# Optimization experiments

Measured on AMD Instinct MI355X. Metric: run time of the kernel, lower is better.

## Reference

```python
import jax, jax.numpy as jnp
import numpy as np

B, L, E, S = 4, 1024, 256, 32  # batch, seq_len, e_dim, local window half-size
NEG = -1e30  # stands in for excluding out-of-range positions from softmax


def setup_inputs() -> dict:
    key = jax.random.key(0)
    ks = jax.random.split(key, 8)
    sc = 1.0 / np.sqrt(E)
    return {
        "q": jax.random.normal(ks[0], (B, L, E), jnp.float32),
        "Wq": jax.random.normal(ks[1], (E, E), jnp.float32) * sc,
        "bq": jax.random.normal(ks[2], (E,), jnp.float32) * sc,
        "Wk": jax.random.normal(ks[3], (E, E), jnp.float32) * sc,
        "bk": jax.random.normal(ks[4], (E,), jnp.float32) * sc,
        "Wv": jax.random.normal(ks[5], (E, E), jnp.float32) * sc,
        "bv": jax.random.normal(ks[6], (E,), jnp.float32) * sc,
        "pos_bias": jax.random.normal(ks[7], (2 * S + 1, E), jnp.float32),
    }


def reference(q, Wq, bq, Wk, bk, Wv, bv, pos_bias):
    # Linear projections (nn.Linear: x @ W.T + b)
    Q = q @ Wq.T + bq
    K = q @ Wk.T + bk
    V = q @ Wv.T + bv

    W = 2 * S + 1
    rel = jnp.arange(-S, S + 1)                      # [W] relative offsets
    idx = jnp.arange(L)[:, None] + rel[None, :]       # [L, W] absolute positions
    valid = (idx >= 0) & (idx < L)                    # in-sequence window entries
    idxc = jnp.clip(idx, 0, L - 1)
    strict = jnp.abs(rel) < S                         # |j-i| < s mask (zeroes K at edges)

    # Gather windows: [B, L, W, E]
    K_win = K[:, idxc] + pos_bias[rel + S][None, None, :, :]
    K_masked = jnp.where(strict[None, None, :, None], K_win, 0.0)
    # Out-of-range positions excluded from softmax entirely (logit -> -inf)
    logits = jnp.where(valid[None, :, :, None], Q[:, :, None, :] * K_masked, NEG)
    weights = jax.nn.softmax(logits, axis=2)          # per-channel softmax over window

    V_win = jnp.where(valid[None, :, :, None], V[:, idxc], 0.0)
    ctx = jnp.sum(weights * V_win, axis=2)            # [B, L, E]

    sig = jax.nn.sigmoid(Q)
    # sigmoid applied inside the loop and again at the end -> squared
    return sig * sig * ctx
```

## Files before the change

kernel.cpp:

```cpp
#include <hip/hip_runtime.h>
#include <hip/hip_bf16.h>

#define B_ 4
#define L_ 1024
#define E_ 256
#define S_ 32

typedef __bf16 bf16x8 __attribute__((ext_vector_type(8)));
typedef float f32x4 __attribute__((ext_vector_type(4)));

__device__ __forceinline__ __bf16 bf_from_bits(unsigned short u) {
    __bf16 b;
    __builtin_memcpy(&b, &u, 2);
    return b;
}

__device__ __forceinline__ void load8split(const float* __restrict__ p,
                                           bf16x8& h, bf16x8& l) {
    const float4 x0 = *(const float4*)p;
    const float4 x1 = *(const float4*)(p + 4);
    const float xs[8] = {x0.x, x0.y, x0.z, x0.w, x1.x, x1.y, x1.z, x1.w};
#pragma unroll
    for (int j = 0; j < 8; ++j) {
        const unsigned hb = __float_as_uint(xs[j]) & 0xFFFF0000u;
        h[j] = bf_from_bits((unsigned short)(hb >> 16));
        l[j] = (__bf16)(xs[j] - __uint_as_float(hb));
    }
}

__global__ __launch_bounds__(256, 1) void qkv_gemm2(
    const float* __restrict__ A,
    const float* __restrict__ Wq, const float* __restrict__ bq,
    const float* __restrict__ Wk, const float* __restrict__ bk,
    const float* __restrict__ Wv, const float* __restrict__ bv,
    float* __restrict__ Qo, float* __restrict__ Ko, float* __restrict__ Vo)
{
    const float* Wm;
    const float* bm;
    float* Om;
    const int z = blockIdx.z;
    if (z == 0)      { Wm = Wq; bm = bq; Om = Qo; }
    else if (z == 1) { Wm = Wk; bm = bk; Om = Ko; }
    else             { Wm = Wv; bm = bv; Om = Vo; }

    const int wave = threadIdx.x >> 6;
    const int lane = threadIdx.x & 63;
    const int rsel = lane & 15;
    const int koff = (lane >> 4) * 8;

    const int m0 = blockIdx.x * 32;
    const int nb = wave * 64;

    const float* pa0 = A + (size_t)(m0 + rsel) * 256 + koff;
    const float* pa1 = pa0 + (size_t)16 * 256;
    const float* pw0 = Wm + (size_t)(nb + 0  + rsel) * 256 + koff;
    const float* pw1 = Wm + (size_t)(nb + 16 + rsel) * 256 + koff;
    const float* pw2 = Wm + (size_t)(nb + 32 + rsel) * 256 + koff;
    const float* pw3 = Wm + (size_t)(nb + 48 + rsel) * 256 + koff;

    f32x4 acc[2][4];
#pragma unroll
    for (int mt = 0; mt < 2; ++mt)
#pragma unroll
        for (int nt = 0; nt < 4; ++nt)
            acc[mt][nt] = (f32x4){0.f, 0.f, 0.f, 0.f};

#pragma unroll
    for (int k0 = 0; k0 < 256; k0 += 32) {
        bf16x8 ah[2], al[2], bh[4], bl[4];
        load8split(pa0 + k0, ah[0], al[0]);
        load8split(pa1 + k0, ah[1], al[1]);
        load8split(pw0 + k0, bh[0], bl[0]);
        load8split(pw1 + k0, bh[1], bl[1]);
        load8split(pw2 + k0, bh[2], bl[2]);
        load8split(pw3 + k0, bh[3], bl[3]);
#pragma unroll
        for (int mt = 0; mt < 2; ++mt)
#pragma unroll
            for (int nt = 0; nt < 4; ++nt) {
                acc[mt][nt] = __builtin_amdgcn_mfma_f32_16x16x32_bf16(
                    ah[mt], bh[nt], acc[mt][nt], 0, 0, 0);
                acc[mt][nt] = __builtin_amdgcn_mfma_f32_16x16x32_bf16(
                    ah[mt], bl[nt], acc[mt][nt], 0, 0, 0);
                acc[mt][nt] = __builtin_amdgcn_mfma_f32_16x16x32_bf16(
                    al[mt], bh[nt], acc[mt][nt], 0, 0, 0);
            }
    }

#pragma unroll
    for (int mt = 0; mt < 2; ++mt) {
        const int mrow = m0 + mt * 16 + (lane >> 4) * 4;
#pragma unroll
        for (int nt = 0; nt < 4; ++nt) {
            const int n = nb + nt * 16 + rsel;
            const float bias = bm[n];
#pragma unroll
            for (int r = 0; r < 4; ++r)
                Om[(size_t)(mrow + r) * 256 + n] = acc[mt][nt][r] + bias;
        }
    }
}

#define TI2 32
#define CH2 64
#define HB2 96
#define PS2 68

__global__ __launch_bounds__(256) void aft_stage2b(
    const float* __restrict__ Q, const float* __restrict__ K,
    const float* __restrict__ V, const float* __restrict__ pb,
    float* __restrict__ out)
{
    __shared__ float Kw[HB2][PS2];
    __shared__ float Vw[HB2][PS2];
    __shared__ float Pw[2 * S_ + 1][PS2];

    const int tid = threadIdx.x;
    const int b  = blockIdx.y;
    const int i0 = blockIdx.x * TI2;
    const int c0 = blockIdx.z * CH2;

    const float* Kb = K + (size_t)b * L_ * E_;
    const float* Vb = V + (size_t)b * L_ * E_;

    for (int idx = tid; idx < HB2 * 16; idx += 256) {
        const int r  = idx >> 4;
        const int cq = (idx & 15) * 4;
        int j = i0 - S_ + r;
        j = j < 0 ? 0 : (j > L_ - 1 ? L_ - 1 : j);
        const size_t g = (size_t)j * E_ + c0 + cq;
        *(float4*)&Kw[r][cq] = *(const float4*)(Kb + g);
        *(float4*)&Vw[r][cq] = *(const float4*)(Vb + g);
    }
    for (int idx = tid; idx < (2 * S_ + 1) * 16; idx += 256) {
        const int r  = idx >> 4;
        const int cq = (idx & 15) * 4;
        *(float4*)&Pw[r][cq] = *(const float4*)(pb + (size_t)r * E_ + c0 + cq);
    }
    __syncthreads();

    const int cq = (tid & 15) * 4;
    const int is = tid >> 4;

#pragma unroll
    for (int rep = 0; rep < 2; ++rep) {
        const int rr = is + rep * 16;
        const int i  = i0 + rr;

        const float4 qv = *(const float4*)(Q + ((size_t)b * L_ + i) * E_ + c0 + cq);

        float den0 = 0.f, den1 = 0.f, den2 = 0.f, den3 = 0.f;
        float num0 = 0.f, num1 = 0.f, num2 = 0.f, num3 = 0.f;

        const int jlo = (i - S_ < 0) ? 0 : (i - S_);
        const int jhi = (i + S_ > L_ - 1) ? (L_ - 1) : (i + S_);

        for (int j = jlo; j <= jhi; ++j) {
            const int r = j - (i0 - S_);
            const int w = j - i + S_;
            const float4 vv = *(const float4*)&Vw[r][cq];

            float kx = 0.f, ky = 0.f, kz = 0.f, kw = 0.f;
            if (w != 0 && w != 2 * S_) {
                const float4 kk = *(const float4*)&Kw[r][cq];
                const float4 pp = *(const float4*)&Pw[w][cq];
                kx = kk.x + pp.x;
                ky = kk.y + pp.y;
                kz = kk.z + pp.z;
                kw = kk.w + pp.w;
            }
            const float e0 = __expf(qv.x * kx);
            const float e1 = __expf(qv.y * ky);
            const float e2 = __expf(qv.z * kz);
            const float e3 = __expf(qv.w * kw);
            den0 += e0; den1 += e1; den2 += e2; den3 += e3;
            num0 += e0 * vv.x; num1 += e1 * vv.y;
            num2 += e2 * vv.z; num3 += e3 * vv.w;
        }

        const float s0 = 1.f / (1.f + __expf(-qv.x));
        const float s1 = 1.f / (1.f + __expf(-qv.y));
        const float s2 = 1.f / (1.f + __expf(-qv.z));
        const float s3 = 1.f / (1.f + __expf(-qv.w));

        float4 o;
        o.x = s0 * s0 * num0 / den0;
        o.y = s1 * s1 * num1 / den1;
        o.z = s2 * s2 * num2 / den2;
        o.w = s3 * s3 * num3 / den3;
        *(float4*)(out + ((size_t)b * L_ + i) * E_ + c0 + cq) = o;
    }
}

#define TI 32
#define CG 64
#define RK 96
#define LDP 68

__global__ __launch_bounds__(256) void aft_fused(
    const float* __restrict__ q,
    const float* __restrict__ Wq, const float* __restrict__ bq,
    const float* __restrict__ Wk, const float* __restrict__ bk,
    const float* __restrict__ Wv, const float* __restrict__ bv,
    const float* __restrict__ pb,
    float* __restrict__ out)
{
    __shared__ float Kl[RK][LDP];
    __shared__ float Vl[RK][LDP];
    __shared__ float Ql[TI][LDP];

    const int i0 = blockIdx.x * TI;
    const int b  = blockIdx.y;
    const int c0 = blockIdx.z * CG;

    const int wave = threadIdx.x >> 6;
    const int lane = threadIdx.x & 63;
    const int rsel = lane & 15;
    const int koff = (lane >> 4) * 8;

    const float* qb = q + (size_t)b * L_ * E_;

    for (int job = wave; job < 56; job += 4) {
        int p, rt, ct;
        if (job < 24)      { p = 0; rt = job >> 2;        ct = job & 3; }
        else if (job < 48) { p = 1; rt = (job - 24) >> 2; ct = (job - 24) & 3; }
        else               { p = 2; rt = (job - 48) >> 2; ct = (job - 48) & 3; }

        int jrow = (p == 2) ? (i0 + rt * 16 + rsel)
                            : (i0 - S_ + rt * 16 + rsel);
        int jc = jrow < 0 ? 0 : (jrow > L_ - 1 ? L_ - 1 : jrow);
        const float* pa = qb + (size_t)jc * E_ + koff;

        const float* Wm = (p == 0) ? Wk : (p == 1) ? Wv : Wq;
        const float* bm = (p == 0) ? bk : (p == 1) ? bv : bq;
        const int n = c0 + ct * 16 + rsel;
        const float* pw = Wm + (size_t)n * E_ + koff;

        f32x4 acc = {0.f, 0.f, 0.f, 0.f};
#pragma unroll
        for (int k0 = 0; k0 < 256; k0 += 32) {
            bf16x8 ah, al, bh, bl;
            load8split(pa + k0, ah, al);
            load8split(pw + k0, bh, bl);
            acc = __builtin_amdgcn_mfma_f32_16x16x32_bf16(ah, bh, acc, 0, 0, 0);
            acc = __builtin_amdgcn_mfma_f32_16x16x32_bf16(ah, bl, acc, 0, 0, 0);
            acc = __builtin_amdgcn_mfma_f32_16x16x32_bf16(al, bh, acc, 0, 0, 0);
        }

        const float bias = bm[n];
        const int row0 = rt * 16 + (lane >> 4) * 4;
        const int colc = ct * 16 + rsel;
        float* dst = (p == 0) ? &Kl[0][0] : (p == 1) ? &Vl[0][0] : &Ql[0][0];
#pragma unroll
        for (int r = 0; r < 4; ++r)
            dst[(size_t)(row0 + r) * LDP + colc] = acc[r] + bias;
    }
    __syncthreads();

    const int cq  = threadIdx.x & 15;
    const int is0 = threadIdx.x >> 4;
    const int cL  = cq * 4;
    const int cG  = c0 + cL;
    const float* pbc = pb + cG;

    for (int rr = is0; rr < TI; rr += 16) {
        const int i = i0 + rr;
        const float4 qv = *(const float4*)&Ql[rr][cL];

        float den0 = 0.f, den1 = 0.f, den2 = 0.f, den3 = 0.f;
        float num0 = 0.f, num1 = 0.f, num2 = 0.f, num3 = 0.f;

        const int jlo = (i - S_ < 0) ? 0 : (i - S_);
        const int jhi = (i + S_ > L_ - 1) ? (L_ - 1) : (i + S_);

        for (int j = jlo; j <= jhi; ++j) {
            const int r = j - (i0 - S_);
            const int w = j - i + S_;
            const float4 vv = *(const float4*)&Vl[r][cL];

            float kx = 0.f, ky = 0.f, kz = 0.f, kw = 0.f;
            if (w != 0 && w != 2 * S_) {
                const float4 kk = *(const float4*)&Kl[r][cL];
                const float4 pp = *(const float4*)(pbc + (size_t)w * E_);
                kx = kk.x + pp.x;
                ky = kk.y + pp.y;
                kz = kk.z + pp.z;
                kw = kk.w + pp.w;
            }
            const float e0 = __expf(qv.x * kx);
            const float e1 = __expf(qv.y * ky);
            const float e2 = __expf(qv.z * kz);
            const float e3 = __expf(qv.w * kw);
            den0 += e0; den1 += e1; den2 += e2; den3 += e3;
            num0 += e0 * vv.x; num1 += e1 * vv.y;
            num2 += e2 * vv.z; num3 += e3 * vv.w;
        }

        const float s0 = 1.f / (1.f + __expf(-qv.x));
        const float s1 = 1.f / (1.f + __expf(-qv.y));
        const float s2 = 1.f / (1.f + __expf(-qv.z));
        const float s3 = 1.f / (1.f + __expf(-qv.w));

        float4 o;
        o.x = s0 * s0 * num0 / den0;
        o.y = s1 * s1 * num1 / den1;
        o.z = s2 * s2 * num2 / den2;
        o.w = s3 * s3 * num3 / den3;
        *(float4*)(out + ((size_t)b * L_ + i) * E_ + cG) = o;
    }
}

extern "C" void kernel_launch(void* const* d_in, const int* in_sizes, int n_in,
                              void* d_out, int out_size, void* d_ws, size_t ws_size,
                              hipStream_t stream) {
    const float* q  = (const float*)d_in[0];
    const float* Wq = (const float*)d_in[1];
    const float* bq = (const float*)d_in[2];
    const float* Wk = (const float*)d_in[3];
    const float* bk = (const float*)d_in[4];
    const float* Wv = (const float*)d_in[5];
    const float* bv = (const float*)d_in[6];
    const float* pb = (const float*)d_in[7];

    const size_t needA = (size_t)3 * 4096 * 256 * sizeof(float);

    if (ws_size >= needA) {
        float* Qf = (float*)d_ws;
        float* Kf = Qf + (size_t)4096 * 256;
        float* Vf = Kf + (size_t)4096 * 256;
        qkv_gemm2<<<dim3(128, 1, 3), 256, 0, stream>>>(q, Wq, bq, Wk, bk, Wv, bv,
                                                       Qf, Kf, Vf);
        aft_stage2b<<<dim3(L_ / TI2, B_, E_ / CH2), 256, 0, stream>>>(
            Qf, Kf, Vf, pb, (float*)d_out);
    } else {
        aft_fused<<<dim3(L_ / TI, B_, E_ / CG), 256, 0, stream>>>(
            q, Wq, bq, Wk, bk, Wv, bv, pb, (float*)d_out);
    }
}
```

Measured before the change: 124.4 us.

## Hoist strict-edge terms out of window loop and halve channel tile

The attention stage now handles the two edge window entries (w=0 and w=2S), whose masked K gives exp(0)=1, in closed form before the loop. An interior fast path then iterates only over the strict window with no per-iteration branch or bounds check, while edge rows take a masked path. The channel tile is halved so each thread handles one row, giving twice as many blocks, less LDS per block and a launch-bounds occupancy hint. The cost is reloading K/V halos across more blocks.

New measurement: 119.2 us. 1.04x faster.

```diff
diff --git a/kernel.cpp b/kernel.cpp
--- a/kernel.cpp
+++ b/kernel.cpp
@@ -101,95 +101,106 @@
     }
 }
 
-#define TI2 32
-#define CH2 64
-#define HB2 96
-#define PS2 68
-
-__global__ __launch_bounds__(256) void aft_stage2b(
+#define TI3 32
+#define CH3 32
+#define HB3 96
+#define PS3 36
+
+__global__ __launch_bounds__(256, 4) void aft_stage2c(
     const float* __restrict__ Q, const float* __restrict__ K,
     const float* __restrict__ V, const float* __restrict__ pb,
     float* __restrict__ out)
 {
-    __shared__ float Kw[HB2][PS2];
-    __shared__ float Vw[HB2][PS2];
-    __shared__ float Pw[2 * S_ + 1][PS2];
+    __shared__ float Kw[HB3][PS3];
+    __shared__ float Vw[HB3][PS3];
+    __shared__ float Pw[2 * S_ + 1][PS3];
 
     const int tid = threadIdx.x;
     const int b  = blockIdx.y;
-    const int i0 = blockIdx.x * TI2;
-    const int c0 = blockIdx.z * CH2;
+    const int i0 = blockIdx.x * TI3;
+    const int c0 = blockIdx.z * CH3;
+
+    const int cq = (tid & 7) * 4;
+    const int rr = tid >> 3;
+    const int i  = i0 + rr;
+
+    const float4 qv = *(const float4*)(Q + ((size_t)b * L_ + i) * E_ + c0 + cq);
 
     const float* Kb = K + (size_t)b * L_ * E_;
     const float* Vb = V + (size_t)b * L_ * E_;
 
-    for (int idx = tid; idx < HB2 * 16; idx += 256) {
-        const int r  = idx >> 4;
-        const int cq = (idx & 15) * 4;
+    for (int idx = tid; idx < HB3 * 8; idx += 256) {
+        const int r = idx >> 3;
+        const int c = (idx & 7) * 4;
         int j = i0 - S_ + r;
         j = j < 0 ? 0 : (j > L_ - 1 ? L_ - 1 : j);
-        const size_t g = (size_t)j * E_ + c0 + cq;
-        *(float4*)&Kw[r][cq] = *(const float4*)(Kb + g);
-        *(float4*)&Vw[r][cq] = *(const float4*)(Vb + g);
-    }
-    for (int idx = tid; idx < (2 * S_ + 1) * 16; idx += 256) {
-        const int r  = idx >> 4;
-        const int cq = (idx & 15) * 4;
-        *(float4*)&Pw[r][cq] = *(const float4*)(pb + (size_t)r * E_ + c0 + cq);
+        const size_t g = (size_t)j * E_ + c0 + c;
+        *(float4*)&Kw[r][c] = *(const float4*)(Kb + g);
+        *(float4*)&Vw[r][c] = *(const float4*)(Vb + g);
+    }
+    for (int idx = tid; idx < (2 * S_ + 1) * 8; idx += 256) {
+        const int r = idx >> 3;
+        const int c = (idx & 7) * 4;
+        *(float4*)&Pw[r][c] = *(const float4*)(pb + (size_t)r * E_ + c0 + c);
     }
     __syncthreads();
 
-    const int cq = (tid & 15) * 4;
-    const int is = tid >> 4;
-
-#pragma unroll
-    for (int rep = 0; rep < 2; ++rep) {
-        const int rr = is + rep * 16;
-        const int i  = i0 + rr;
-
-        const float4 qv = *(const float4*)(Q + ((size_t)b * L_ + i) * E_ + c0 + cq);
-
-        float den0 = 0.f, den1 = 0.f, den2 = 0.f, den3 = 0.f;
-        float num0 = 0.f, num1 = 0.f, num2 = 0.f, num3 = 0.f;
-
-        const int jlo = (i - S_ < 0) ? 0 : (i - S_);
-        const int jhi = (i + S_ > L_ - 1) ? (L_ - 1) : (i + S_);
-
-        for (int j = jlo; j <= jhi; ++j) {
-            const int r = j - (i0 - S_);
-            const int w = j - i + S_;
+    const float mA = (i >= S_) ? 1.f : 0.f;
+    const float mB = (i <= L_ - 1 - S_) ? 1.f : 0.f;
+    const float4 vA = *(const float4*)&Vw[rr][cq];
+    const float4 vB = *(const float4*)&Vw[rr + 2 * S_][cq];
+
+    float den0 = mA + mB, den1 = mA + mB, den2 = mA + mB, den3 = mA + mB;
+    float num0 = mA * vA.x + mB * vB.x;
+    float num1 = mA * vA.y + mB * vB.y;
+    float num2 = mA * vA.z + mB * vB.z;
+    float num3 = mA * vA.w + mB * vB.w;
+
+    if (i >= S_ - 1 && i <= L_ - S_) {
+#pragma unroll 7
+        for (int w = 1; w < 2 * S_; ++w) {
+            const int r = rr + w;
+            const float4 kk = *(const float4*)&Kw[r][cq];
+            const float4 pp = *(const float4*)&Pw[w][cq];
             const float4 vv = *(const float4*)&Vw[r][cq];
-
-            float kx = 0.f, ky = 0.f, kz = 0.f, kw = 0.f;
-            if (w != 0 && w != 2 * S_) {
-                const float4 kk = *(const float4*)&Kw[r][cq];
-                const float4 pp = *(const float4*)&Pw[w][cq];
-                kx = kk.x + pp.x;
-                ky = kk.y + pp.y;
-                kz = kk.z + pp.z;
-                kw = kk.w + pp.w;
-            }
-            const float e0 = __expf(qv.x * kx);
-            const float e1 = __expf(qv.y * ky);
-            const float e2 = __expf(qv.z * kz);
-            const float e3 = __expf(qv.w * kw);
+            const float e0 = __expf(qv.x * (kk.x + pp.x));
+            const float e1 = __expf(qv.y * (kk.y + pp.y));
+            const float e2 = __expf(qv.z * (kk.z + pp.z));
+            const float e3 = __expf(qv.w * (kk.w + pp.w));
             den0 += e0; den1 += e1; den2 += e2; den3 += e3;
             num0 += e0 * vv.x; num1 += e1 * vv.y;
             num2 += e2 * vv.z; num3 += e3 * vv.w;
         }
-
-        const float s0 = 1.f / (1.f + __expf(-qv.x));
-        const float s1 = 1.f / (1.f + __expf(-qv.y));
-        const float s2 = 1.f / (1.f + __expf(-qv.z));
-        const float s3 = 1.f / (1.f + __expf(-qv.w));
-
-        float4 o;
-        o.x = s0 * s0 * num0 / den0;
-        o.y = s1 * s1 * num1 / den1;
-        o.z = s2 * s2 * num2 / den2;
-        o.w = s3 * s3 * num3 / den3;
-        *(float4*)(out + ((size_t)b * L_ + i) * E_ + c0 + cq) = o;
-    }
+    } else {
+#pragma unroll 7
+        for (int w = 1; w < 2 * S_; ++w) {
+            const int r = rr + w;
+            const int j = i - S_ + w;
+            const float m = (j >= 0 && j <= L_ - 1) ? 1.f : 0.f;
+            const float4 kk = *(const float4*)&Kw[r][cq];
+            const float4 pp = *(const float4*)&Pw[w][cq];
+            const float4 vv = *(const float4*)&Vw[r][cq];
+            const float e0 = m * __expf(qv.x * (kk.x + pp.x));
+            const float e1 = m * __expf(qv.y * (kk.y + pp.y));
+            const float e2 = m * __expf(qv.z * (kk.z + pp.z));
+            const float e3 = m * __expf(qv.w * (kk.w + pp.w));
+            den0 += e0; den1 += e1; den2 += e2; den3 += e3;
+            num0 += e0 * vv.x; num1 += e1 * vv.y;
+            num2 += e2 * vv.z; num3 += e3 * vv.w;
+        }
+    }
+
+    const float s0 = 1.f / (1.f + __expf(-qv.x));
+    const float s1 = 1.f / (1.f + __expf(-qv.y));
+    const float s2 = 1.f / (1.f + __expf(-qv.z));
+    const float s3 = 1.f / (1.f + __expf(-qv.w));
+
+    float4 o;
+    o.x = s0 * s0 * num0 / den0;
+    o.y = s1 * s1 * num1 / den1;
+    o.z = s2 * s2 * num2 / den2;
+    o.w = s3 * s3 * num3 / den3;
+    *(float4*)(out + ((size_t)b * L_ + i) * E_ + c0 + cq) = o;
 }
 
 #define TI 32
@@ -330,7 +341,7 @@
         float* Vf = Kf + (size_t)4096 * 256;
         qkv_gemm2<<<dim3(128, 1, 3), 256, 0, stream>>>(q, Wq, bq, Wk, bk, Wv, bv,
                                                        Qf, Kf, Vf);
-        aft_stage2b<<<dim3(L_ / TI2, B_, E_ / CH2), 256, 0, stream>>>(
+        aft_stage2c<<<dim3(L_ / TI3, B_, E_ / CH3), 256, 0, stream>>>(
             Qf, Kf, Vf, pb, (float*)d_out);
     } else {
         aft_fused<<<dim3(L_ / TI, B_, E_ / CG), 256, 0, stream>>>(
```

## Rewrite windowed softmax stage with paired rows, shared K/V loads and interior fast path

Applied to the files above, without the earlier changes.

Replaces the second-stage local-attention kernel with one where each thread handles two adjacent query rows over two channels. The rows share K and V loads from LDS, and the positional bias is rolled forward in a register, cutting LDS traffic per exponential. Edge window entries with zeroed K are folded in as exp(0)=1 constants. Interior blocks take a branch-free path, while boundary blocks use a validity multiplier instead of data-dependent loop bounds. It also switches to exp2f with a log2e-prescaled Q, halves the channel tile to double the grid size, and adds an occupancy hint, at the cost of more code.

After: 122.4 us. Within noise of the previous version (-1.6%).

```diff
diff --git a/kernel.cpp b/kernel.cpp
--- a/kernel.cpp
+++ b/kernel.cpp
@@ -101,95 +101,165 @@
     }
 }
 
-#define TI2 32
-#define CH2 64
-#define HB2 96
-#define PS2 68
-
-__global__ __launch_bounds__(256) void aft_stage2b(
+#define TI5 32
+#define CH5 32
+#define HR5 96
+#define PS5 36
+
+__global__ __launch_bounds__(256, 4) void aft_stage2e(
     const float* __restrict__ Q, const float* __restrict__ K,
     const float* __restrict__ V, const float* __restrict__ pb,
     float* __restrict__ out)
 {
-    __shared__ float Kw[HB2][PS2];
-    __shared__ float Vw[HB2][PS2];
-    __shared__ float Pw[2 * S_ + 1][PS2];
+    __shared__ float Kw[HR5][PS5];
+    __shared__ float Vw[HR5][PS5];
+    __shared__ float Pw[2 * S_ + 1][PS5];
 
     const int tid = threadIdx.x;
     const int b  = blockIdx.y;
-    const int i0 = blockIdx.x * TI2;
-    const int c0 = blockIdx.z * CH2;
+    const int i0 = blockIdx.x * TI5;
+    const int c0 = blockIdx.z * CH5;
+
+    const int duo = tid & 15;
+    const int pr  = tid >> 4;
+    const int c   = duo * 2;
+    const int iA  = i0 + pr * 2;
+    const int iB  = iA + 1;
+    const int rb  = pr * 2;
+
+    const float2 qA = *(const float2*)(Q + ((size_t)b * L_ + iA) * E_ + c0 + c);
+    const float2 qB = *(const float2*)(Q + ((size_t)b * L_ + iB) * E_ + c0 + c);
 
     const float* Kb = K + (size_t)b * L_ * E_;
     const float* Vb = V + (size_t)b * L_ * E_;
 
-    for (int idx = tid; idx < HB2 * 16; idx += 256) {
-        const int r  = idx >> 4;
-        const int cq = (idx & 15) * 4;
+    for (int idx = tid; idx < HR5 * 8; idx += 256) {
+        const int r = idx >> 3;
+        const int cc = (idx & 7) * 4;
         int j = i0 - S_ + r;
         j = j < 0 ? 0 : (j > L_ - 1 ? L_ - 1 : j);
-        const size_t g = (size_t)j * E_ + c0 + cq;
-        *(float4*)&Kw[r][cq] = *(const float4*)(Kb + g);
-        *(float4*)&Vw[r][cq] = *(const float4*)(Vb + g);
-    }
-    for (int idx = tid; idx < (2 * S_ + 1) * 16; idx += 256) {
-        const int r  = idx >> 4;
-        const int cq = (idx & 15) * 4;
-        *(float4*)&Pw[r][cq] = *(const float4*)(pb + (size_t)r * E_ + c0 + cq);
+        const size_t g = (size_t)j * E_ + c0 + cc;
+        *(float4*)&Kw[r][cc] = *(const float4*)(Kb + g);
+        *(float4*)&Vw[r][cc] = *(const float4*)(Vb + g);
+    }
+    for (int idx = tid; idx < (2 * S_ + 1) * 8; idx += 256) {
+        const int r = idx >> 3;
+        const int cc = (idx & 7) * 4;
+        *(float4*)&Pw[r][cc] = *(const float4*)(pb + (size_t)r * E_ + c0 + cc);
     }
     __syncthreads();
 
-    const int cq = (tid & 15) * 4;
-    const int is = tid >> 4;
-
-#pragma unroll
-    for (int rep = 0; rep < 2; ++rep) {
-        const int rr = is + rep * 16;
-        const int i  = i0 + rr;
-
-        const float4 qv = *(const float4*)(Q + ((size_t)b * L_ + i) * E_ + c0 + cq);
-
-        float den0 = 0.f, den1 = 0.f, den2 = 0.f, den3 = 0.f;
-        float num0 = 0.f, num1 = 0.f, num2 = 0.f, num3 = 0.f;
-
-        const int jlo = (i - S_ < 0) ? 0 : (i - S_);
-        const int jhi = (i + S_ > L_ - 1) ? (L_ - 1) : (i + S_);
-
-        for (int j = jlo; j <= jhi; ++j) {
-            const int r = j - (i0 - S_);
-            const int w = j - i + S_;
-            const float4 vv = *(const float4*)&Vw[r][cq];
-
-            float kx = 0.f, ky = 0.f, kz = 0.f, kw = 0.f;
-            if (w != 0 && w != 2 * S_) {
-                const float4 kk = *(const float4*)&Kw[r][cq];
-                const float4 pp = *(const float4*)&Pw[w][cq];
-                kx = kk.x + pp.x;
-                ky = kk.y + pp.y;
-                kz = kk.z + pp.z;
-                kw = kk.w + pp.w;
-            }
-            const float e0 = __expf(qv.x * kx);
-            const float e1 = __expf(qv.y * ky);
-            const float e2 = __expf(qv.z * kz);
-            const float e3 = __expf(qv.w * kw);
-            den0 += e0; den1 += e1; den2 += e2; den3 += e3;
-            num0 += e0 * vv.x; num1 += e1 * vv.y;
-            num2 += e2 * vv.z; num3 += e3 * vv.w;
-        }
-
-        const float s0 = 1.f / (1.f + __expf(-qv.x));
-        const float s1 = 1.f / (1.f + __expf(-qv.y));
-        const float s2 = 1.f / (1.f + __expf(-qv.z));
-        const float s3 = 1.f / (1.f + __expf(-qv.w));
-
-        float4 o;
-        o.x = s0 * s0 * num0 / den0;
-        o.y = s1 * s1 * num1 / den1;
-        o.z = s2 * s2 * num2 / den2;
-        o.w = s3 * s3 * num3 / den3;
-        *(float4*)(out + ((size_t)b * L_ + i) * E_ + c0 + cq) = o;
-    }
+    const float LOG2E = 1.44269504088896340736f;
+    const float qsA0 = qA.x * LOG2E, qsA1 = qA.y * LOG2E;
+    const float qsB0 = qB.x * LOG2E, qsB1 = qB.y * LOG2E;
+
+    float dA0, dA1, nA0, nA1, dB0, dB1, nB0, nB1;
+
+    {
+        const float m = (iA >= S_) ? 1.f : 0.f;
+        const float2 vv = *(const float2*)&Vw[rb][c];
+        dA0 = m; dA1 = m; nA0 = m * vv.x; nA1 = m * vv.y;
+    }
+    {
+        const float m = (iB <= L_ - 1 - S_) ? 1.f : 0.f;
+        const float2 vv = *(const float2*)&Vw[rb + 65][c];
+        dB0 = m; dB1 = m; nB0 = m * vv.x; nB1 = m * vv.y;
+    }
+
+    float2 ppRoll;
+
+    const bool interior = (blockIdx.x >= 1) && (blockIdx.x <= (L_ / TI5) - 2);
+
+    if (interior) {
+        {
+            const int r = rb + 1;
+            const float2 kk = *(const float2*)&Kw[r][c];
+            const float2 pp = *(const float2*)&Pw[1][c];
+            const float2 vv = *(const float2*)&Vw[r][c];
+            const float a0 = exp2f(qsA0 * (kk.x + pp.x));
+            const float a1 = exp2f(qsA1 * (kk.y + pp.y));
+            dA0 += a0; nA0 += a0 * vv.x; dA1 += a1; nA1 += a1 * vv.y;
+            dB0 += 1.f; nB0 += vv.x;     dB1 += 1.f; nB1 += vv.y;
+            ppRoll = pp;
+        }
+#pragma unroll 8
+        for (int t = 1; t <= 62; ++t) {
+            const int r = rb + 1 + t;
+            const float2 kk = *(const float2*)&Kw[r][c];
+            const float2 pp = *(const float2*)&Pw[t + 1][c];
+            const float2 vv = *(const float2*)&Vw[r][c];
+            const float a0 = exp2f(qsA0 * (kk.x + pp.x));
+            const float a1 = exp2f(qsA1 * (kk.y + pp.y));
+            const float b0 = exp2f(qsB0 * (kk.x + ppRoll.x));
+            const float b1 = exp2f(qsB1 * (kk.y + ppRoll.y));
+            dA0 += a0; nA0 += a0 * vv.x; dA1 += a1; nA1 += a1 * vv.y;
+            dB0 += b0; nB0 += b0 * vv.x; dB1 += b1; nB1 += b1 * vv.y;
+            ppRoll = pp;
+        }
+        {
+            const int r = rb + 64;
+            const float2 kk = *(const float2*)&Kw[r][c];
+            const float2 vv = *(const float2*)&Vw[r][c];
+            const float b0 = exp2f(qsB0 * (kk.x + ppRoll.x));
+            const float b1 = exp2f(qsB1 * (kk.y + ppRoll.y));
+            dB0 += b0; nB0 += b0 * vv.x; dB1 += b1; nB1 += b1 * vv.y;
+            dA0 += 1.f; nA0 += vv.x;     dA1 += 1.f; nA1 += vv.y;
+        }
+    } else {
+        {
+            const int j = iA - S_ + 1;
+            const float m = (j >= 0 && j <= L_ - 1) ? 1.f : 0.f;
+            const int r = rb + 1;
+            const float2 kk = *(const float2*)&Kw[r][c];
+            const float2 pp = *(const float2*)&Pw[1][c];
+            const float2 vv = *(const float2*)&Vw[r][c];
+            const float a0 = m * exp2f(qsA0 * (kk.x + pp.x));
+            const float a1 = m * exp2f(qsA1 * (kk.y + pp.y));
+            dA0 += a0; nA0 += a0 * vv.x; dA1 += a1; nA1 += a1 * vv.y;
+            dB0 += m;  nB0 += m * vv.x;  dB1 += m;  nB1 += m * vv.y;
+            ppRoll = pp;
+        }
+#pragma unroll 8
+        for (int t = 1; t <= 62; ++t) {
+            const int j = iA - S_ + 1 + t;
+            const float m = (j >= 0 && j <= L_ - 1) ? 1.f : 0.f;
+            const int r = rb + 1 + t;
+            const float2 kk = *(const float2*)&Kw[r][c];
+            const float2 pp = *(const float2*)&Pw[t + 1][c];
+            const float2 vv = *(const float2*)&Vw[r][c];
+            const float a0 = m * exp2f(qsA0 * (kk.x + pp.x));
+            const float a1 = m * exp2f(qsA1 * (kk.y + pp.y));
+            const float b0 = m * exp2f(qsB0 * (kk.x + ppRoll.x));
+            const float b1 = m * exp2f(qsB1 * (kk.y + ppRoll.y));
+            dA0 += a0; nA0 += a0 * vv.x; dA1 += a1; nA1 += a1 * vv.y;
+            dB0 += b0; nB0 += b0 * vv.x; dB1 += b1; nB1 += b1 * vv.y;
+            ppRoll = pp;
+        }
+        {
+            const int j = iA + S_;
+            const float m = (j >= 0 && j <= L_ - 1) ? 1.f : 0.f;
+            const int r = rb + 64;
+            const float2 kk = *(const float2*)&Kw[r][c];
+            const float2 vv = *(const float2*)&Vw[r][c];
+            const float b0 = m * exp2f(qsB0 * (kk.x + ppRoll.x));
+            const float b1 = m * exp2f(qsB1 * (kk.y + ppRoll.y));
+            dB0 += b0; nB0 += b0 * vv.x; dB1 += b1; nB1 += b1 * vv.y;
+            dA0 += m;  nA0 += m * vv.x;  dA1 += m;  nA1 += m * vv.y;
+        }
+    }
+
+    const float sA0 = 1.f / (1.f + exp2f(-qsA0));
+    const float sA1 = 1.f / (1.f + exp2f(-qsA1));
+    const float sB0 = 1.f / (1.f + exp2f(-qsB0));
+    const float sB1 = 1.f / (1.f + exp2f(-qsB1));
+
+    float2 oA, oB;
+    oA.x = sA0 * sA0 * nA0 / dA0;
+    oA.y = sA1 * sA1 * nA1 / dA1;
+    oB.x = sB0 * sB0 * nB0 / dB0;
+    oB.y = sB1 * sB1 * nB1 / dB1;
+    *(float2*)(out + ((size_t)b * L_ + iA) * E_ + c0 + c) = oA;
+    *(float2*)(out + ((size_t)b * L_ + iB) * E_ + c0 + c) = oB;
 }
 
 #define TI 32
@@ -330,7 +400,7 @@
         float* Vf = Kf + (size_t)4096 * 256;
         qkv_gemm2<<<dim3(128, 1, 3), 256, 0, stream>>>(q, Wq, bq, Wk, bk, Wv, bv,
                                                        Qf, Kf, Vf);
-        aft_stage2b<<<dim3(L_ / TI2, B_, E_ / CH2), 256, 0, stream>>>(
+        aft_stage2e<<<dim3(L_ / TI5, B_, E_ / CH5), 256, 0, stream>>>(
             Qf, Kf, Vf, pb, (float*)d_out);
     } else {
         aft_fused<<<dim3(L_ / TI, B_, E_ / CG), 256, 0, stream>>>(
```

## Register-block four rows per thread in windowed softmax stage with rotating pos-bias

Applied to the files above, without the earlier changes.

Replaces the stage-2 windowed softmax kernel with one where each thread handles four consecutive rows and two channels. Each K/V row loaded from LDS is reused across the four output rows, and pos-bias values rotate through registers. Interior blocks get a branch-free path where edge window entries contribute exp(0)=1 directly, while boundary blocks use a multiplicative mask. Exponentials switch to exp2 with a pre-scaled q, and the launch uses 128-thread blocks over narrower channel chunks. The cost is higher register pressure and more code.

Result: faster. 114.5 us (-8.0%).

```diff
diff --git a/kernel.cpp b/kernel.cpp
--- a/kernel.cpp
+++ b/kernel.cpp
@@ -13,6 +13,14 @@
     __bf16 b;
     __builtin_memcpy(&b, &u, 2);
     return b;
+}
+
+__device__ __forceinline__ float fexp2(float x) {
+#if __has_builtin(__builtin_amdgcn_exp2f)
+    return __builtin_amdgcn_exp2f(x);
+#else
+    return exp2f(x);
+#endif
 }
 
 __device__ __forceinline__ void load8split(const float* __restrict__ p,
@@ -101,95 +109,320 @@
     }
 }
 
-#define TI2 32
-#define CH2 64
-#define HB2 96
-#define PS2 68
-
-__global__ __launch_bounds__(256) void aft_stage2b(
+#define TI7 32
+#define CH7 32
+#define HR7 96
+#define PS7 36
+
+#define STEP4I(T, PNEW, PH1, PH2, PH3)                                   \
+    {                                                                    \
+        const int rl = rb + (T);                                         \
+        const float2 kk = *(const float2*)&Kw[rl][c];                    \
+        const float2 vv = *(const float2*)&Vw[rl][c];                    \
+        PNEW = *(const float2*)&Pw[(T)][c];                              \
+        const float e0x = fexp2(qs0x * (kk.x + PNEW.x));                 \
+        const float e0y = fexp2(qs0y * (kk.y + PNEW.y));                 \
+        const float e1x = fexp2(qs1x * (kk.x + PH1.x));                  \
+        const float e1y = fexp2(qs1y * (kk.y + PH1.y));                  \
+        const float e2x = fexp2(qs2x * (kk.x + PH2.x));                  \
+        const float e2y = fexp2(qs2y * (kk.y + PH2.y));                  \
+        const float e3x = fexp2(qs3x * (kk.x + PH3.x));                  \
+        const float e3y = fexp2(qs3y * (kk.y + PH3.y));                  \
+        d0x += e0x; n0x += e0x * vv.x; d0y += e0y; n0y += e0y * vv.y;    \
+        d1x += e1x; n1x += e1x * vv.x; d1y += e1y; n1y += e1y * vv.y;    \
+        d2x += e2x; n2x += e2x * vv.x; d2y += e2y; n2y += e2y * vv.y;    \
+        d3x += e3x; n3x += e3x * vv.x; d3y += e3y; n3y += e3y * vv.y;    \
+    }
+
+#define STEP4E(T, PNEW, PH1, PH2, PH3)                                   \
+    {                                                                    \
+        const int jj = iA - S_ + (T);                                    \
+        const float m = (jj >= 0 && jj <= L_ - 1) ? 1.f : 0.f;           \
+        const int rl = rb + (T);                                         \
+        const float2 kk = *(const float2*)&Kw[rl][c];                    \
+        const float2 vv = *(const float2*)&Vw[rl][c];                    \
+        PNEW = *(const float2*)&Pw[(T)][c];                              \
+        const float e0x = m * fexp2(qs0x * (kk.x + PNEW.x));             \
+        const float e0y = m * fexp2(qs0y * (kk.y + PNEW.y));             \
+        const float e1x = m * fexp2(qs1x * (kk.x + PH1.x));              \
+        const float e1y = m * fexp2(qs1y * (kk.y + PH1.y));              \
+        const float e2x = m * fexp2(qs2x * (kk.x + PH2.x));              \
+        const float e2y = m * fexp2(qs2y * (kk.y + PH2.y));              \
+        const float e3x = m * fexp2(qs3x * (kk.x + PH3.x));              \
+        const float e3y = m * fexp2(qs3y * (kk.y + PH3.y));              \
+        d0x += e0x; n0x += e0x * vv.x; d0y += e0y; n0y += e0y * vv.y;    \
+        d1x += e1x; n1x += e1x * vv.x; d1y += e1y; n1y += e1y * vv.y;    \
+        d2x += e2x; n2x += e2x * vv.x; d2y += e2y; n2y += e2y * vv.y;    \
+        d3x += e3x; n3x += e3x * vv.x; d3y += e3y; n3y += e3y * vv.y;    \
+    }
+
+__global__ __launch_bounds__(128, 2) void aft_stage2g(
     const float* __restrict__ Q, const float* __restrict__ K,
     const float* __restrict__ V, const float* __restrict__ pb,
     float* __restrict__ out)
 {
-    __shared__ float Kw[HB2][PS2];
-    __shared__ float Vw[HB2][PS2];
-    __shared__ float Pw[2 * S_ + 1][PS2];
+    __shared__ float Kw[HR7][PS7];
+    __shared__ float Vw[HR7][PS7];
+    __shared__ float Pw[2 * S_ + 1][PS7];
 
     const int tid = threadIdx.x;
     const int b  = blockIdx.y;
-    const int i0 = blockIdx.x * TI2;
-    const int c0 = blockIdx.z * CH2;
+    const int i0 = blockIdx.x * TI7;
+    const int c0 = blockIdx.z * CH7;
+
+    const int duo = tid & 15;
+    const int qd  = tid >> 4;
+    const int c   = duo * 2;
+    const int iA  = i0 + qd * 4;
+    const int rb  = qd * 4;
+
+    const float* Qr = Q + ((size_t)b * L_ + iA) * E_ + c0 + c;
+    const float2 qv0 = *(const float2*)(Qr);
+    const float2 qv1 = *(const float2*)(Qr + E_);
+    const float2 qv2 = *(const float2*)(Qr + 2 * E_);
+    const float2 qv3 = *(const float2*)(Qr + 3 * E_);
 
     const float* Kb = K + (size_t)b * L_ * E_;
     const float* Vb = V + (size_t)b * L_ * E_;
 
-    for (int idx = tid; idx < HB2 * 16; idx += 256) {
-        const int r  = idx >> 4;
-        const int cq = (idx & 15) * 4;
+    for (int idx = tid; idx < HR7 * 8; idx += 128) {
+        const int r = idx >> 3;
+        const int cc = (idx & 7) * 4;
         int j = i0 - S_ + r;
         j = j < 0 ? 0 : (j > L_ - 1 ? L_ - 1 : j);
-        const size_t g = (size_t)j * E_ + c0 + cq;
-        *(float4*)&Kw[r][cq] = *(const float4*)(Kb + g);
-        *(float4*)&Vw[r][cq] = *(const float4*)(Vb + g);
-    }
-    for (int idx = tid; idx < (2 * S_ + 1) * 16; idx += 256) {
-        const int r  = idx >> 4;
-        const int cq = (idx & 15) * 4;
-        *(float4*)&Pw[r][cq] = *(const float4*)(pb + (size_t)r * E_ + c0 + cq);
+        const size_t g = (size_t)j * E_ + c0 + cc;
+        *(float4*)&Kw[r][cc] = *(const float4*)(Kb + g);
+        *(float4*)&Vw[r][cc] = *(const float4*)(Vb + g);
+    }
+    for (int idx = tid; idx < (2 * S_ + 1) * 8; idx += 128) {
+        const int r = idx >> 3;
+        const int cc = (idx & 7) * 4;
+        *(float4*)&Pw[r][cc] = *(const float4*)(pb + (size_t)r * E_ + c0 + cc);
     }
     __syncthreads();
 
-    const int cq = (tid & 15) * 4;
-    const int is = tid >> 4;
-
-#pragma unroll
-    for (int rep = 0; rep < 2; ++rep) {
-        const int rr = is + rep * 16;
-        const int i  = i0 + rr;
-
-        const float4 qv = *(const float4*)(Q + ((size_t)b * L_ + i) * E_ + c0 + cq);
-
-        float den0 = 0.f, den1 = 0.f, den2 = 0.f, den3 = 0.f;
-        float num0 = 0.f, num1 = 0.f, num2 = 0.f, num3 = 0.f;
-
-        const int jlo = (i - S_ < 0) ? 0 : (i - S_);
-        const int jhi = (i + S_ > L_ - 1) ? (L_ - 1) : (i + S_);
-
-        for (int j = jlo; j <= jhi; ++j) {
-            const int r = j - (i0 - S_);
-            const int w = j - i + S_;
-            const float4 vv = *(const float4*)&Vw[r][cq];
-
-            float kx = 0.f, ky = 0.f, kz = 0.f, kw = 0.f;
-            if (w != 0 && w != 2 * S_) {
-                const float4 kk = *(const float4*)&Kw[r][cq];
-                const float4 pp = *(const float4*)&Pw[w][cq];
-                kx = kk.x + pp.x;
-                ky = kk.y + pp.y;
-                kz = kk.z + pp.z;
-                kw = kk.w + pp.w;
-            }
-            const float e0 = __expf(qv.x * kx);
-            const float e1 = __expf(qv.y * ky);
-            const float e2 = __expf(qv.z * kz);
-            const float e3 = __expf(qv.w * kw);
-            den0 += e0; den1 += e1; den2 += e2; den3 += e3;
-            num0 += e0 * vv.x; num1 += e1 * vv.y;
-            num2 += e2 * vv.z; num3 += e3 * vv.w;
-        }
-
-        const float s0 = 1.f / (1.f + __expf(-qv.x));
-        const float s1 = 1.f / (1.f + __expf(-qv.y));
-        const float s2 = 1.f / (1.f + __expf(-qv.z));
-        const float s3 = 1.f / (1.f + __expf(-qv.w));
-
-        float4 o;
-        o.x = s0 * s0 * num0 / den0;
-        o.y = s1 * s1 * num1 / den1;
-        o.z = s2 * s2 * num2 / den2;
-        o.w = s3 * s3 * num3 / den3;
-        *(float4*)(out + ((size_t)b * L_ + i) * E_ + c0 + cq) = o;
-    }
+    const float LOG2E = 1.44269504088896340736f;
+    const float qs0x = qv0.x * LOG2E, qs0y = qv0.y * LOG2E;
+    const float qs1x = qv1.x * LOG2E, qs1y = qv1.y * LOG2E;
+    const float qs2x = qv2.x * LOG2E, qs2y = qv2.y * LOG2E;
+    const float qs3x = qv3.x * LOG2E, qs3y = qv3.y * LOG2E;
+
+    float d0x = 0.f, d0y = 0.f, n0x = 0.f, n0y = 0.f;
+    float d1x = 0.f, d1y = 0.f, n1x = 0.f, n1y = 0.f;
+    float d2x = 0.f, d2y = 0.f, n2x = 0.f, n2y = 0.f;
+    float d3x = 0.f, d3y = 0.f, n3x = 0.f, n3y = 0.f;
+
+    float2 p0, h1, h2, h3;
+
+    const bool interior = (blockIdx.x >= 1) && (blockIdx.x <= (L_ / TI7) - 2);
+
+    if (interior) {
+        {
+            const float2 vv = *(const float2*)&Vw[rb][c];
+            d0x += 1.f; n0x += vv.x; d0y += 1.f; n0y += vv.y;
+        }
+        {
+            const float2 kk = *(const float2*)&Kw[rb + 1][c];
+            const float2 vv = *(const float2*)&Vw[rb + 1][c];
+            h3 = *(const float2*)&Pw[1][c];
+            const float e0x = fexp2(qs0x * (kk.x + h3.x));
+            const float e0y = fexp2(qs0y * (kk.y + h3.y));
+            d0x += e0x; n0x += e0x * vv.x; d0y += e0y; n0y += e0y * vv.y;
+            d1x += 1.f; n1x += vv.x;       d1y += 1.f; n1y += vv.y;
+        }
+        {
+            const float2 kk = *(const float2*)&Kw[rb + 2][c];
+            const float2 vv = *(const float2*)&Vw[rb + 2][c];
+            h2 = *(const float2*)&Pw[2][c];
+            const float e0x = fexp2(qs0x * (kk.x + h2.x));
+            const float e0y = fexp2(qs0y * (kk.y + h2.y));
+            const float e1x = fexp2(qs1x * (kk.x + h3.x));
+            const float e1y = fexp2(qs1y * (kk.y + h3.y));
+            d0x += e0x; n0x += e0x * vv.x; d0y += e0y; n0y += e0y * vv.y;
+            d1x += e1x; n1x += e1x * vv.x; d1y += e1y; n1y += e1y * vv.y;
+            d2x += 1.f; n2x += vv.x;       d2y += 1.f; n2y += vv.y;
+        }
+        {
+            const float2 kk = *(const float2*)&Kw[rb + 3][c];
+            const float2 vv = *(const float2*)&Vw[rb + 3][c];
+            h1 = *(const float2*)&Pw[3][c];
+            const float e0x = fexp2(qs0x * (kk.x + h1.x));
+            const float e0y = fexp2(qs0y * (kk.y + h1.y));
+            const float e1x = fexp2(qs1x * (kk.x + h2.x));
+            const float e1y = fexp2(qs1y * (kk.y + h2.y));
+            const float e2x = fexp2(qs2x * (kk.x + h3.x));
+            const float e2y = fexp2(qs2y * (kk.y + h3.y));
+            d0x += e0x; n0x += e0x * vv.x; d0y += e0y; n0y += e0y * vv.y;
+            d1x += e1x; n1x += e1x * vv.x; d1y += e1y; n1y += e1y * vv.y;
+            d2x += e2x; n2x += e2x * vv.x; d2y += e2y; n2y += e2y * vv.y;
+            d3x += 1.f; n3x += vv.x;       d3y += 1.f; n3y += vv.y;
+        }
+#pragma unroll 2
+        for (int t = 4; t <= 60; t += 4) {
+            STEP4I(t + 0, p0, h1, h2, h3)
+            STEP4I(t + 1, h3, p0, h1, h2)
+            STEP4I(t + 2, h2, h3, p0, h1)
+            STEP4I(t + 3, h1, h2, h3, p0)
+        }
+        {
+            const float2 kk = *(const float2*)&Kw[rb + 64][c];
+            const float2 vv = *(const float2*)&Vw[rb + 64][c];
+            const float e1x = fexp2(qs1x * (kk.x + h1.x));
+            const float e1y = fexp2(qs1y * (kk.y + h1.y));
+            const float e2x = fexp2(qs2x * (kk.x + h2.x));
+            const float e2y = fexp2(qs2y * (kk.y + h2.y));
+            const float e3x = fexp2(qs3x * (kk.x + h3.x));
+            const float e3y = fexp2(qs3y * (kk.y + h3.y));
+            d0x += 1.f; n0x += vv.x;       d0y += 1.f; n0y += vv.y;
+            d1x += e1x; n1x += e1x * vv.x; d1y += e1y; n1y += e1y * vv.y;
+            d2x += e2x; n2x += e2x * vv.x; d2y += e2y; n2y += e2y * vv.y;
+            d3x += e3x; n3x += e3x * vv.x; d3y += e3y; n3y += e3y * vv.y;
+        }
+        {
+            const float2 kk = *(const float2*)&Kw[rb + 65][c];
+            const float2 vv = *(const float2*)&Vw[rb + 65][c];
+            const float e2x = fexp2(qs2x * (kk.x + h1.x));
+            const float e2y = fexp2(qs2y * (kk.y + h1.y));
+            const float e3x = fexp2(qs3x * (kk.x + h2.x));
+            const float e3y = fexp2(qs3y * (kk.y + h2.y));
+            d1x += 1.f; n1x += vv.x;       d1y += 1.f; n1y += vv.y;
+            d2x += e2x; n2x += e2x * vv.x; d2y += e2y; n2y += e2y * vv.y;
+            d3x += e3x; n3x += e3x * vv.x; d3y += e3y; n3y += e3y * vv.y;
+        }
+        {
+            const float2 kk = *(const float2*)&Kw[rb + 66][c];
+            const float2 vv = *(const float2*)&Vw[rb + 66][c];
+            const float e3x = fexp2(qs3x * (kk.x + h1.x));
+            const float e3y = fexp2(qs3y * (kk.y + h1.y));
+            d2x += 1.f; n2x += vv.x;       d2y += 1.f; n2y += vv.y;
+            d3x += e3x; n3x += e3x * vv.x; d3y += e3y; n3y += e3y * vv.y;
+        }
+        {
+            const float2 vv = *(const float2*)&Vw[rb + 67][c];
+            d3x += 1.f; n3x += vv.x; d3y += 1.f; n3y += vv.y;
+        }
+    } else {
+        {
+            const int jj = iA - S_;
+            const float m = (jj >= 0) ? 1.f : 0.f;
+            const float2 vv = *(const float2*)&Vw[rb][c];
+            d0x += m; n0x += m * vv.x; d0y += m; n0y += m * vv.y;
+        }
+        {
+            const int jj = iA - S_ + 1;
+            const float m = (jj >= 0 && jj <= L_ - 1) ? 1.f : 0.f;
+            const float2 kk = *(const float2*)&Kw[rb + 1][c];
+            const float2 vv = *(const float2*)&Vw[rb + 1][c];
+            h3 = *(const float2*)&Pw[1][c];
+            const float e0x = m * fexp2(qs0x * (kk.x + h3.x));
+            const float e0y = m * fexp2(qs0y * (kk.y + h3.y));
+            d0x += e0x; n0x += e0x * vv.x; d0y += e0y; n0y += e0y * vv.y;
+            d1x += m;   n1x += m * vv.x;   d1y += m;   n1y += m * vv.y;
+        }
+        {
+            const int jj = iA - S_ + 2;
+            const float m = (jj >= 0 && jj <= L_ - 1) ? 1.f : 0.f;
+            const float2 kk = *(const float2*)&Kw[rb + 2][c];
+            const float2 vv = *(const float2*)&Vw[rb + 2][c];
+            h2 = *(const float2*)&Pw[2][c];
+            const float e0x = m * fexp2(qs0x * (kk.x + h2.x));
+            const float e0y = m * fexp2(qs0y * (kk.y + h2.y));
+            const float e1x = m * fexp2(qs1x * (kk.x + h3.x));
+            const float e1y = m * fexp2(qs1y * (kk.y + h3.y));
+            d0x += e0x; n0x += e0x * vv.x; d0y += e0y; n0y += e0y * vv.y;
+            d1x += e1x; n1x += e1x * vv.x; d1y += e1y; n1y += e1y * vv.y;
+            d2x += m;   n2x += m * vv.x;   d2y += m;   n2y += m * vv.y;
+        }
+        {
+            const int jj = iA - S_ + 3;
+            const float m = (jj >= 0 && jj <= L_ - 1) ? 1.f : 0.f;
+            const float2 kk = *(const float2*)&Kw[rb + 3][c];
+            const float2 vv = *(const float2*)&Vw[rb + 3][c];
+            h1 = *(const float2*)&Pw[3][c];
+            const float e0x = m * fexp2(qs0x * (kk.x + h1.x));
+            const float e0y = m * fexp2(qs0y * (kk.y + h1.y));
+            const float e1x = m * fexp2(qs1x * (kk.x + h2.x));
+            const float e1y = m * fexp2(qs1y * (kk.y + h2.y));
+            const float e2x = m * fexp2(qs2x * (kk.x + h3.x));
+            const float e2y = m * fexp2(qs2y * (kk.y + h3.y));
+            d0x += e0x; n0x += e0x * vv.x; d0y += e0y; n0y += e0y * vv.y;
+            d1x += e1x; n1x += e1x * vv.x; d1y += e1y; n1y += e1y * vv.y;
+            d2x += e2x; n2x += e2x * vv.x; d2y += e2y; n2y += e2y * vv.y;
+            d3x += m;   n3x += m * vv.x;   d3y += m;   n3y += m * vv.y;
+        }
+#pragma unroll 2
+        for (int t = 4; t <= 60; t += 4) {
+            STEP4E(t + 0, p0, h1, h2, h3)
+            STEP4E(t + 1, h3, p0, h1, h2)
+            STEP4E(t + 2, h2, h3, p0, h1)
+            STEP4E(t + 3, h1, h2, h3, p0)
+        }
+        {
+            const int jj = iA - S_ + 64;
+            const float m = (jj >= 0 && jj <= L_ - 1) ? 1.f : 0.f;
+            const float2 kk = *(const float2*)&Kw[rb + 64][c];
+            const float2 vv = *(const float2*)&Vw[rb + 64][c];
+            const float e1x = m * fexp2(qs1x * (kk.x + h1.x));
+            const float e1y = m * fexp2(qs1y * (kk.y + h1.y));
+            const float e2x = m * fexp2(qs2x * (kk.x + h2.x));
+            const float e2y = m * fexp2(qs2y * (kk.y + h2.y));
+            const float e3x = m * fexp2(qs3x * (kk.x + h3.x));
+            const float e3y = m * fexp2(qs3y * (kk.y + h3.y));
+            d0x += m;   n0x += m * vv.x;   d0y += m;   n0y += m * vv.y;
+            d1x += e1x; n1x += e1x * vv.x; d1y += e1y; n1y += e1y * vv.y;
+            d2x += e2x; n2x += e2x * vv.x; d2y += e2y; n2y += e2y * vv.y;
+            d3x += e3x; n3x += e3x * vv.x; d3y += e3y; n3y += e3y * vv.y;
+        }
+        {
+            const int jj = iA - S_ + 65;
+            const float m = (jj >= 0 && jj <= L_ - 1) ? 1.f : 0.f;
+            const float2 kk = *(const float2*)&Kw[rb + 65][c];
+            const float2 vv = *(const float2*)&Vw[rb + 65][c];
+            const float e2x = m * fexp2(qs2x * (kk.x + h1.x));
+            const float e2y = m * fexp2(qs2y * (kk.y + h1.y));
+            const float e3x = m * fexp2(qs3x * (kk.x + h2.x));
+            const float e3y = m * fexp2(qs3y * (kk.y + h2.y));
+            d1x += m;   n1x += m * vv.x;   d1y += m;   n1y += m * vv.y;
+            d2x += e2x; n2x += e2x * vv.x; d2y += e2y; n2y += e2y * vv.y;
+            d3x += e3x; n3x += e3x * vv.x; d3y += e3y; n3y += e3y * vv.y;
+        }
+        {
+            const int jj = iA - S_ + 66;
+            const float m = (jj >= 0 && jj <= L_ - 1) ? 1.f : 0.f;
+            const float2 kk = *(const float2*)&Kw[rb + 66][c];
+            const float2 vv = *(const float2*)&Vw[rb + 66][c];
+            const float e3x = m * fexp2(qs3x * (kk.x + h1.x));
+            const float e3y = m * fexp2(qs3y * (kk.y + h1.y));
+            d2x += m;   n2x += m * vv.x;   d2y += m;   n2y += m * vv.y;
+            d3x += e3x; n3x += e3x * vv.x; d3y += e3y; n3y += e3y * vv.y;
+        }
+        {
+            const int jj = iA - S_ + 67;
+            const float m = (jj >= 0 && jj <= L_ - 1) ? 1.f : 0.f;
+            const float2 vv = *(const float2*)&Vw[rb + 67][c];
+            d3x += m; n3x += m * vv.x; d3y += m; n3y += m * vv.y;
+        }
+    }
+
+    const float s0x = 1.f / (1.f + fexp2(-qs0x));
+    const float s0y = 1.f / (1.f + fexp2(-qs0y));
+    const float s1x = 1.f / (1.f + fexp2(-qs1x));
+    const float s1y = 1.f / (1.f + fexp2(-qs1y));
+    const float s2x = 1.f / (1.f + fexp2(-qs2x));
+    const float s2y = 1.f / (1.f + fexp2(-qs2y));
+    const float s3x = 1.f / (1.f + fexp2(-qs3x));
+    const float s3y = 1.f / (1.f + fexp2(-qs3y));
+
+    float* ob = out + ((size_t)b * L_ + iA) * E_ + c0 + c;
+    float2 o;
+    o.x = s0x * s0x * n0x / d0x; o.y = s0y * s0y * n0y / d0y;
+    *(float2*)(ob) = o;
+    o.x = s1x * s1x * n1x / d1x; o.y = s1y * s1y * n1y / d1y;
+    *(float2*)(ob + E_) = o;
+    o.x = s2x * s2x * n2x / d2x; o.y = s2y * s2y * n2y / d2y;
+    *(float2*)(ob + 2 * E_) = o;
+    o.x = s3x * s3x * n3x / d3x; o.y = s3y * s3y * n3y / d3y;
+    *(float2*)(ob + 3 * E_) = o;
 }
 
 #define TI 32
@@ -330,7 +563,7 @@
         float* Vf = Kf + (size_t)4096 * 256;
         qkv_gemm2<<<dim3(128, 1, 3), 256, 0, stream>>>(q, Wq, bq, Wk, bk, Wv, bv,
                                                        Qf, Kf, Vf);
-        aft_stage2b<<<dim3(L_ / TI2, B_, E_ / CH2), 256, 0, stream>>>(
+        aft_stage2g<<<dim3(L_ / TI7, B_, E_ / CH7), 128, 0, stream>>>(
             Qf, Kf, Vf, pb, (float*)d_out);
     } else {
         aft_fused<<<dim3(L_ / TI, B_, E_ / CG), 256, 0, stream>>>(
```
